# Optimization experiments

Hardware: AMD Instinct MI355X
Metric: run time of the kernel (lower is better)

Reference implementation:

```python
import jax, jax.numpy as jnp
import numpy as np

N_NODES = 50000


def _sage_conv(x, src, dst, Wl, Wr, b):
    # mean aggregation of source-node features onto targets (PyG SAGEConv, aggr='mean')
    msg = x[src]                                              # [E, d]
    agg = jax.ops.segment_sum(msg, dst, num_segments=N_NODES)  # [N, d]
    cnt = jax.ops.segment_sum(jnp.ones((src.shape[0],), x.dtype), dst, num_segments=N_NODES)
    mean = agg / jnp.maximum(cnt, 1.0)[:, None]
    return mean @ Wl + x @ Wr + b


def _layer_norm(x, g, b, eps=1e-5):
    mu = jnp.mean(x, axis=-1, keepdims=True)
    var = jnp.var(x, axis=-1, keepdims=True)
    return (x - mu) * jax.lax.rsqrt(var + eps) * g + b


def setup_inputs() -> dict:
    key = jax.random.key(0)
    ks = jax.random.split(key, 10)
    d_in, d_h, d_out = 128, 128, 2
    scale_h = 1.0 / np.sqrt(d_in)
    x = jax.random.normal(ks[0], (N_NODES, d_in), jnp.float32)
    edge_index = jax.random.randint(ks[1], (2, 800000), 0, N_NODES, dtype=jnp.int64)
    return {
        "x": x,
        "edge_index": edge_index,
        "W1l": jax.random.normal(ks[2], (d_in, d_h), jnp.float32) * scale_h,
        "W1r": jax.random.normal(ks[3], (d_in, d_h), jnp.float32) * scale_h,
        "b1": jnp.zeros((d_h,), jnp.float32),
        "ln1_g": jnp.ones((d_h,), jnp.float32),
        "ln1_b": jnp.zeros((d_h,), jnp.float32),
        "W2l": jax.random.normal(ks[4], (d_h, d_h), jnp.float32) * scale_h,
        "W2r": jax.random.normal(ks[5], (d_h, d_h), jnp.float32) * scale_h,
        "b2": jnp.zeros((d_h,), jnp.float32),
        "ln2_g": jnp.ones((d_h,), jnp.float32),
        "ln2_b": jnp.zeros((d_h,), jnp.float32),
        "W3l": jax.random.normal(ks[6], (d_h, d_out), jnp.float32) * scale_h,
        "W3r": jax.random.normal(ks[7], (d_h, d_out), jnp.float32) * scale_h,
        "b3": jnp.zeros((d_out,), jnp.float32),
    }


def reference(x, edge_index, W1l, W1r, b1, ln1_g, ln1_b, W2l, W2r, b2, ln2_g, ln2_b, W3l, W3r, b3):
    src, dst = edge_index[0], edge_index[1]
    h = _sage_conv(x, src, dst, W1l, W1r, b1)
    h = jax.nn.relu(_layer_norm(h, ln1_g, ln1_b))
    h = _sage_conv(h, src, dst, W2l, W2r, b2)
    h = jax.nn.relu(_layer_norm(h, ln2_g, ln2_b))
    return _sage_conv(h, src, dst, W3l, W3r, b3)
```

## Files before the change

kernel.cpp:

```cpp
#include <hip/hip_runtime.h>

#define N_NODES 50000
#define CAP 64
#define NBK 196
#define BCAP2 4608
#define EPB 4096
#define PB ((int)0xAAAAAAAA)

#define SLS ((size_t)N_NODES * 32)

typedef unsigned int uint;
typedef unsigned short ushort;
typedef __attribute__((ext_vector_type(8))) short bf16x8;
typedef __attribute__((ext_vector_type(4))) float f32x4;

__device__ inline float bf2f(uint u) { u <<= 16; return __builtin_bit_cast(float, u); }
__device__ inline ushort f2bf(float f) {
    uint u = __builtin_bit_cast(uint, f);
    u = (u + 0x7fffu + ((u >> 16) & 1u)) >> 16;
    return (ushort)u;
}


__global__ __launch_bounds__(256) void k_prep(
    const int* __restrict__ src, const int* __restrict__ dst, int E,
    int* __restrict__ bcnt, uint* __restrict__ bstage,
    const float* __restrict__ x, ushort* __restrict__ Xb, int n8,
    const float* __restrict__ W1l, const float* __restrict__ W1r, ushort* __restrict__ Wp1,
    const float* __restrict__ W2l, const float* __restrict__ W2r, ushort* __restrict__ Wp2,
    int bBin, int bC) {
    __shared__ uint recs[EPB];
    __shared__ int hist[NBK], base[NBK], cursor[NBK], gbase[NBK];
    __shared__ int ws[4];
    int b = blockIdx.x, t = threadIdx.x;
    if (b < bBin) {
        int i0 = b * EPB;
        for (int i = t; i < NBK; i += 256) hist[i] = 0;
        __syncthreads();
        uint r[16];
#pragma unroll
        for (int k = 0; k < 16; ++k) {
            int i = i0 + k * 256 + t;
            if (i < E) {
                int s = src[i], d = dst[i];
                r[k] = ((uint)s << 16) | (uint)d;
                atomicAdd(&hist[d >> 8], 1);
            } else r[k] = 0xffffffffu;
        }
        __syncthreads();
        int lane = t & 63, w = t >> 6;
        int v = (t < NBK) ? hist[t] : 0;
        int xsc = v;
#pragma unroll
        for (int o = 1; o < 64; o <<= 1) {
            int y = __shfl_up(xsc, o, 64);
            if (lane >= o) xsc += y;
        }
        if (lane == 63) ws[w] = xsc;
        __syncthreads();
        int add = 0;
        for (int k = 0; k < 4; ++k)
            if (k < w) add += ws[k];
        if (t < NBK) { base[t] = xsc - v + add; cursor[t] = xsc - v + add; }
        __syncthreads();
#pragma unroll
        for (int k = 0; k < 16; ++k) {
            if (r[k] != 0xffffffffu) {
                int bk = (int)((r[k] & 0xffffu) >> 8);
                int pos = atomicAdd(&cursor[bk], 1);
                recs[pos] = r[k];
            }
        }
        __syncthreads();
        for (int i = t; i < NBK; i += 256) {
            int h = hist[i];
            gbase[i] = h ? (atomicAdd(&bcnt[i], h) - PB) : 0;
        }
        __syncthreads();
        int mblk = min(E - i0, EPB);
        for (int i = t; i < mblk; i += 256) {
            uint rr = recs[i];
            int bk = (int)((rr & 0xffffu) >> 8);
            int pos = gbase[bk] + (i - base[bk]);
            if (pos < BCAP2) bstage[(size_t)bk * BCAP2 + pos] = rr;
        }
    } else if (b < bBin + bC) {
        int i = (b - bBin) * 256 + t;
        if (i < n8) {
            int node = i >> 4, f8 = i & 15;
            const float4* xp = (const float4*)(x + (size_t)node * 128 + f8 * 8);
            float4 v0 = xp[0], v1 = xp[1];
            uint4 o;
            o.x = (uint)f2bf(v0.x) | ((uint)f2bf(v0.y) << 16);
            o.y = (uint)f2bf(v0.z) | ((uint)f2bf(v0.w) << 16);
            o.z = (uint)f2bf(v1.x) | ((uint)f2bf(v1.y) << 16);
            o.w = (uint)f2bf(v1.z) | ((uint)f2bf(v1.w) << 16);
            *(uint4*)(Xb + (size_t)(f8 >> 2) * SLS + (size_t)node * 32 + (f8 & 3) * 8) = o;
        }
    } else if (b < bBin + bC + 128) {
        int idx = (b - bBin - bC) * 256 + t;
        int k = idx >> 7, n = idx & 127;
        float v = (k < 128) ? W1l[k * 128 + n] : W1r[(k - 128) * 128 + n];
        Wp1[((k >> 3) << 10) + (n << 3) + (k & 7)] = f2bf(v);
    } else {
        int idx = (b - bBin - bC - 128) * 256 + t;
        int k = idx >> 7, n = idx & 127;
        float v = (k < 128) ? W2l[k * 128 + n] : W2r[(k - 128) * 128 + n];
        Wp2[((k >> 3) << 10) + (n << 3) + (k & 7)] = f2bf(v);
    }
}


__global__ __launch_bounds__(256) void k_csr_build(const int* __restrict__ bcnt,
                                                   const uint* __restrict__ bstage,
                                                   int* __restrict__ cnt,
                                                   ushort* __restrict__ csr, int N) {
    __shared__ int lcnt[256];
    __shared__ ushort lcsr[256 * CAP];
    int b = blockIdx.x, t = threadIdx.x;
    lcnt[t] = 0;
    __syncthreads();
    int m = min(bcnt[b] - PB, BCAP2);
    const uint* st = bstage + (size_t)b * BCAP2;
    for (int i = t; i < m; i += 256) {
        uint rr = st[i];
        int local = rr & 255;
        int slot = atomicAdd(&lcnt[local], 1);
        if (slot < CAP) lcsr[local * CAP + slot] = (ushort)(rr >> 16);
    }
    __syncthreads();
    uint4* d4 = (uint4*)(csr + (size_t)b * 256 * CAP);
    const uint4* s4 = (const uint4*)lcsr;
    for (int i = t; i < 256 * CAP * 2 / 16; i += 256) d4[i] = s4[i];
    int node = b * 256 + t;
    if (node < N) cnt[node] = min(lcnt[t], CAP);
}


__global__ __launch_bounds__(256) void k_agg(const ushort* __restrict__ X,
                                             const int* __restrict__ cnt,
                                             const ushort* __restrict__ csr,
                                             ushort* __restrict__ M, int N) {
    int slice = blockIdx.x & 3;
    int nb = blockIdx.x >> 2;
    int lane = threadIdx.x & 63, wave = threadIdx.x >> 6;
    int es = lane >> 2, fl = lane & 3;
    int node = nb * 64 + wave * 16 + es;
    int end = (node < N) ? cnt[node] : 0;
    int md = end;
    md = max(md, __shfl_xor(md, 4));
    md = max(md, __shfl_xor(md, 8));
    md = max(md, __shfl_xor(md, 16));
    md = max(md, __shfl_xor(md, 32));
    const ushort* rp = csr + (size_t)node * CAP;
    const ushort* Xs = X + (size_t)slice * SLS + fl * 8;
    float a0 = 0.f, a1 = 0.f, a2 = 0.f, a3 = 0.f;
    float a4 = 0.f, a5 = 0.f, a6 = 0.f, a7 = 0.f;
#pragma unroll 4
    for (int e = 0; e < md; ++e) {
        if (e < end) {
            int s = rp[e];
            uint4 v = *(const uint4*)(Xs + (size_t)s * 32);
            a0 += bf2f(v.x); a1 += bf2f(v.x >> 16);
            a2 += bf2f(v.y); a3 += bf2f(v.y >> 16);
            a4 += bf2f(v.z); a5 += bf2f(v.z >> 16);
            a6 += bf2f(v.w); a7 += bf2f(v.w >> 16);
        }
    }
    if (node < N) {
        float inv = 1.0f / (float)max(end, 1);
        uint4 o;
        o.x = (uint)f2bf(a0 * inv) | ((uint)f2bf(a1 * inv) << 16);
        o.y = (uint)f2bf(a2 * inv) | ((uint)f2bf(a3 * inv) << 16);
        o.z = (uint)f2bf(a4 * inv) | ((uint)f2bf(a5 * inv) << 16);
        o.w = (uint)f2bf(a6 * inv) | ((uint)f2bf(a7 * inv) << 16);
        *(uint4*)(M + (size_t)slice * SLS + (size_t)node * 32 + fl * 8) = o;
    }
}


__global__ __launch_bounds__(256, 2) void k_gemm_ln_relu(
    const ushort* __restrict__ Mb, const ushort* __restrict__ Xb,
    const ushort* __restrict__ Wp, const float* __restrict__ bias,
    const float* __restrict__ g, const float* __restrict__ bb,
    ushort* __restrict__ H, int N,
    const float* __restrict__ W3l, const float* __restrict__ W3r,
    const float* __restrict__ b3, float* __restrict__ tb, float* __restrict__ rb) {
    __shared__ ushort sW[256 * 128];
    int tid = threadIdx.x;
    int wave = tid >> 6, lane = tid & 63;
    int l15 = lane & 15, q = lane >> 4;
    int rowBase = blockIdx.x * 64 + wave * 16;
    int arow = rowBase + l15;
    if (arow >= N) arow = N - 1;

    {
        const uint4* wsrc = (const uint4*)Wp;
        uint4* wdst = (uint4*)sW;
#pragma unroll
        for (int i = 0; i < 16; ++i) wdst[i * 256 + tid] = wsrc[i * 256 + tid];
    }

    f32x4 acc[8];
#pragma unroll
    for (int t = 0; t < 8; ++t) acc[t] = (f32x4){0.f, 0.f, 0.f, 0.f};

    const ushort* aM = Mb + (size_t)arow * 32 + q * 8;
    const ushort* aX = Xb + (size_t)arow * 32 + q * 8;
    __syncthreads();
    const ushort* wq = sW + q * 1024 + l15 * 8;

#pragma unroll
    for (int s = 0; s < 8; ++s) {
        bf16x8 a = (s < 4) ? *(const bf16x8*)(aM + (size_t)s * SLS)
                           : *(const bf16x8*)(aX + (size_t)(s - 4) * SLS);
        const ushort* wbase = wq + s * 4096;
#pragma unroll
        for (int t = 0; t < 8; ++t) {
            bf16x8 b = *(const bf16x8*)(wbase + t * 128);
            acc[t] = __builtin_amdgcn_mfma_f32_16x16x32_bf16(a, b, acc[t], 0, 0, 0);
        }
    }

    const bool doProj = (tb != nullptr);
    float gj[8], bbj[8], bj[8];
    float wl0[8], wl1[8], wr0[8], wr1[8];
#pragma unroll
    for (int t = 0; t < 8; ++t) {
        int col = t * 16 + l15;
        gj[t] = g[col]; bbj[t] = bb[col]; bj[t] = bias[col];
    }
    if (doProj) {
#pragma unroll
        for (int t = 0; t < 8; ++t) {
            int col = t * 16 + l15;
            float2 a = *(const float2*)(W3l + col * 2);
            float2 c2 = *(const float2*)(W3r + col * 2);
            wl0[t] = a.x; wl1[t] = a.y; wr0[t] = c2.x; wr1[t] = c2.y;
        }
    }

#pragma unroll
    for (int r = 0; r < 4; ++r) {
        float c[8];
        float s = 0.f, ss = 0.f;
#pragma unroll
        for (int t = 0; t < 8; ++t) {
            c[t] = acc[t][r] + bj[t];
            s += c[t];
            ss += c[t] * c[t];
        }
        s += __shfl_xor(s, 1); ss += __shfl_xor(ss, 1);
        s += __shfl_xor(s, 2); ss += __shfl_xor(ss, 2);
        s += __shfl_xor(s, 4); ss += __shfl_xor(ss, 4);
        s += __shfl_xor(s, 8); ss += __shfl_xor(ss, 8);
        float mu = s * (1.0f / 128.0f);
        float var = ss * (1.0f / 128.0f) - mu * mu;
        float rsig = rsqrtf(var + 1e-5f);
        int node = rowBase + q * 4 + r;
        float y[8];
#pragma unroll
        for (int t = 0; t < 8; ++t) {
            float v = (c[t] - mu) * rsig * gj[t] + bbj[t];
            y[t] = fmaxf(v, 0.f);
        }
        if (!doProj) {
            if (node < N) {
                ushort* hp = H + (size_t)node * 32;
#pragma unroll
                for (int t = 0; t < 8; ++t)
                    hp[(size_t)(t >> 1) * SLS + (t & 1) * 16 + l15] = f2bf(y[t]);
            }
        } else {
            float t0 = 0.f, t1 = 0.f, r0 = 0.f, r1 = 0.f;
#pragma unroll
            for (int t = 0; t < 8; ++t) {
                t0 += y[t] * wl0[t];
                t1 += y[t] * wl1[t];
                r0 += y[t] * wr0[t];
                r1 += y[t] * wr1[t];
            }
#pragma unroll
            for (int o = 1; o < 16; o <<= 1) {
                t0 += __shfl_xor(t0, o);
                t1 += __shfl_xor(t1, o);
                r0 += __shfl_xor(r0, o);
                r1 += __shfl_xor(r1, o);
            }
            if (l15 == 0 && node < N) {
                tb[node * 2 + 0] = t0;
                tb[node * 2 + 1] = t1;
                rb[node * 2 + 0] = r0 + b3[0];
                rb[node * 2 + 1] = r1 + b3[1];
            }
        }
    }
}


__global__ __launch_bounds__(256) void k_final(const float* __restrict__ t, const float* __restrict__ r,
                                               const int* __restrict__ cnt, const ushort* __restrict__ csr,
                                               float* __restrict__ out, int N) {
    int n = blockIdx.x * blockDim.x + threadIdx.x;
    if (n >= N) return;
    int end = cnt[n];
    const ushort* row = csr + (size_t)n * CAP;
    float a0 = 0.f, a1 = 0.f, b0 = 0.f, b1 = 0.f;
    int e = 0;
    for (; e + 3 < end; e += 4) {
        float2 v0 = *(const float2*)(t + row[e] * 2);
        float2 v1 = *(const float2*)(t + row[e + 1] * 2);
        float2 v2 = *(const float2*)(t + row[e + 2] * 2);
        float2 v3 = *(const float2*)(t + row[e + 3] * 2);
        a0 += v0.x + v1.x; a1 += v0.y + v1.y;
        b0 += v2.x + v3.x; b1 += v2.y + v3.y;
    }
    for (; e < end; ++e) {
        float2 v = *(const float2*)(t + row[e] * 2);
        a0 += v.x; a1 += v.y;
    }
    a0 += b0; a1 += b1;
    float inv = 1.0f / (float)max(end, 1);
    out[n * 2 + 0] = a0 * inv + r[n * 2 + 0];
    out[n * 2 + 1] = a1 * inv + r[n * 2 + 1];
}


extern "C" void kernel_launch(void* const* d_in, const int* in_sizes, int n_in,
                              void* d_out, int out_size, void* d_ws, size_t ws_size,
                              hipStream_t stream) {
    const float* x   = (const float*)d_in[0];
    const int* eidx  = (const int*)d_in[1];
    const float* W1l = (const float*)d_in[2];
    const float* W1r = (const float*)d_in[3];
    const float* b1  = (const float*)d_in[4];
    const float* g1  = (const float*)d_in[5];
    const float* bb1 = (const float*)d_in[6];
    const float* W2l = (const float*)d_in[7];
    const float* W2r = (const float*)d_in[8];
    const float* b2  = (const float*)d_in[9];
    const float* g2  = (const float*)d_in[10];
    const float* bb2 = (const float*)d_in[11];
    const float* W3l = (const float*)d_in[12];
    const float* W3r = (const float*)d_in[13];
    const float* b3  = (const float*)d_in[14];
    float* out = (float*)d_out;

    const int N = N_NODES;
    const int E = in_sizes[1] / 2;
    const int* src = eidx;
    const int* dst = eidx + E;

    char* ws = (char*)d_ws;
    size_t off = 0;
    auto alloc = [&](size_t bytes) -> char* {
        char* p = ws + off;
        off += (bytes + 255) & ~(size_t)255;
        return p;
    };
    int* bcnt    = (int*)alloc((size_t)NBK * sizeof(int));
    uint* bstage = (uint*)alloc((size_t)NBK * BCAP2 * sizeof(uint));
    int* cnt     = (int*)alloc((size_t)N * sizeof(int));
    ushort* csr  = (ushort*)alloc((size_t)NBK * 256 * CAP * sizeof(ushort));
    ushort* Xb   = (ushort*)alloc((size_t)N * 128 * sizeof(ushort));
    ushort* Mb   = (ushort*)alloc((size_t)N * 128 * sizeof(ushort));
    ushort* Hb   = (ushort*)alloc((size_t)N * 128 * sizeof(ushort));
    ushort* Wp1  = (ushort*)alloc((size_t)256 * 128 * sizeof(ushort));
    ushort* Wp2  = (ushort*)alloc((size_t)256 * 128 * sizeof(ushort));
    float* tbuf  = (float*)alloc((size_t)N * 2 * sizeof(float));
    float* rbuf  = (float*)alloc((size_t)N * 2 * sizeof(float));

    const int n8 = N * 16;
    const int bBin = (E + EPB - 1) / EPB;
    const int bC = (n8 + 255) / 256;

    k_prep<<<bBin + bC + 256, 256, 0, stream>>>(src, dst, E, bcnt, bstage, x, Xb, n8,
                                                W1l, W1r, Wp1, W2l, W2r, Wp2, bBin, bC);
    k_csr_build<<<NBK, 256, 0, stream>>>(bcnt, bstage, cnt, csr, N);

    const int aggGrid = 4 * ((N + 63) / 64);
    k_agg<<<aggGrid, 256, 0, stream>>>(Xb, cnt, csr, Mb, N);
    k_gemm_ln_relu<<<(N + 63) / 64, 256, 0, stream>>>(Mb, Xb, Wp1, b1, g1, bb1, Hb, N,
                                                      nullptr, nullptr, nullptr, nullptr, nullptr);
    k_agg<<<aggGrid, 256, 0, stream>>>(Hb, cnt, csr, Mb, N);
    k_gemm_ln_relu<<<(N + 63) / 64, 256, 0, stream>>>(Mb, Hb, Wp2, b2, g2, bb2, nullptr, N,
                                                      W3l, W3r, b3, tbuf, rbuf);
    k_final<<<(N + 255) / 256, 256, 0, stream>>>(tbuf, rbuf, cnt, csr, out, N);
}
```

Before: 251.9 us.

## Split each node's neighbor list across four lanes in mean aggregation

```diff
diff --git a/kernel.cpp b/kernel.cpp
--- a/kernel.cpp
+++ b/kernel.cpp
@@ -8,11 +8,13 @@
 #define PB ((int)0xAAAAAAAA)
 
 #define SLS ((size_t)N_NODES * 32)
+#define RS 72
 
 typedef unsigned int uint;
 typedef unsigned short ushort;
 typedef __attribute__((ext_vector_type(8))) short bf16x8;
 typedef __attribute__((ext_vector_type(4))) float f32x4;
+typedef __attribute__((ext_vector_type(4))) uint u32x4;
 
 __device__ inline float bf2f(uint u) { u <<= 16; return __builtin_bit_cast(float, u); }
 __device__ inline ushort f2bf(float f) {
@@ -141,40 +143,68 @@
                                              const int* __restrict__ cnt,
                                              const ushort* __restrict__ csr,
                                              ushort* __restrict__ M, int N) {
+    __shared__ ushort srow[16 * RS];
+    __shared__ int scnt[16];
     int slice = blockIdx.x & 3;
     int nb = blockIdx.x >> 2;
-    int lane = threadIdx.x & 63, wave = threadIdx.x >> 6;
-    int es = lane >> 2, fl = lane & 3;
-    int node = nb * 64 + wave * 16 + es;
-    int end = (node < N) ? cnt[node] : 0;
-    int md = end;
-    md = max(md, __shfl_xor(md, 4));
-    md = max(md, __shfl_xor(md, 8));
-    md = max(md, __shfl_xor(md, 16));
-    md = max(md, __shfl_xor(md, 32));
-    const ushort* rp = csr + (size_t)node * CAP;
+    int node0 = nb * 16;
+    int t = threadIdx.x;
+    if (t < 128) {
+        int ln = t >> 3, c = t & 7;
+        u32x4 v = __builtin_nontemporal_load(
+            (const u32x4*)(csr + (size_t)(node0 + ln) * CAP + c * 8));
+        *(u32x4*)(srow + ln * RS + c * 8) = v;
+        if (c == 0) scnt[ln] = (node0 + ln < N) ? cnt[node0 + ln] : 0;
+    }
+    __syncthreads();
+    int lane = t & 63, wave = t >> 6;
+    int nl = lane >> 4;
+    int es = (lane >> 2) & 3;
+    int fl = lane & 3;
+    int ln = wave * 4 + nl;
+    int node = node0 + ln;
+    int deg = scnt[ln];
+    const ushort* rp = srow + ln * RS;
     const ushort* Xs = X + (size_t)slice * SLS + fl * 8;
     float a0 = 0.f, a1 = 0.f, a2 = 0.f, a3 = 0.f;
     float a4 = 0.f, a5 = 0.f, a6 = 0.f, a7 = 0.f;
-#pragma unroll 4
-    for (int e = 0; e < md; ++e) {
-        if (e < end) {
-            int s = rp[e];
-            uint4 v = *(const uint4*)(Xs + (size_t)s * 32);
-            a0 += bf2f(v.x); a1 += bf2f(v.x >> 16);
-            a2 += bf2f(v.y); a3 += bf2f(v.y >> 16);
-            a4 += bf2f(v.z); a5 += bf2f(v.z >> 16);
-            a6 += bf2f(v.w); a7 += bf2f(v.w >> 16);
-        }
-    }
-    if (node < N) {
-        float inv = 1.0f / (float)max(end, 1);
-        uint4 o;
+    int e = es;
+    for (; e + 4 < deg; e += 8) {
+        int s0 = rp[e], s1 = rp[e + 4];
+        uint4 v0 = *(const uint4*)(Xs + (size_t)s0 * 32);
+        uint4 v1 = *(const uint4*)(Xs + (size_t)s1 * 32);
+        a0 += bf2f(v0.x) + bf2f(v1.x);
+        a1 += bf2f(v0.x >> 16) + bf2f(v1.x >> 16);
+        a2 += bf2f(v0.y) + bf2f(v1.y);
+        a3 += bf2f(v0.y >> 16) + bf2f(v1.y >> 16);
+        a4 += bf2f(v0.z) + bf2f(v1.z);
+        a5 += bf2f(v0.z >> 16) + bf2f(v1.z >> 16);
+        a6 += bf2f(v0.w) + bf2f(v1.w);
+        a7 += bf2f(v0.w >> 16) + bf2f(v1.w >> 16);
+    }
+    if (e < deg) {
+        uint4 v = *(const uint4*)(Xs + (size_t)rp[e] * 32);
+        a0 += bf2f(v.x); a1 += bf2f(v.x >> 16);
+        a2 += bf2f(v.y); a3 += bf2f(v.y >> 16);
+        a4 += bf2f(v.z); a5 += bf2f(v.z >> 16);
+        a6 += bf2f(v.w); a7 += bf2f(v.w >> 16);
+    }
+    a0 += __shfl_xor(a0, 4); a1 += __shfl_xor(a1, 4);
+    a2 += __shfl_xor(a2, 4); a3 += __shfl_xor(a3, 4);
+    a4 += __shfl_xor(a4, 4); a5 += __shfl_xor(a5, 4);
+    a6 += __shfl_xor(a6, 4); a7 += __shfl_xor(a7, 4);
+    a0 += __shfl_xor(a0, 8); a1 += __shfl_xor(a1, 8);
+    a2 += __shfl_xor(a2, 8); a3 += __shfl_xor(a3, 8);
+    a4 += __shfl_xor(a4, 8); a5 += __shfl_xor(a5, 8);
+    a6 += __shfl_xor(a6, 8); a7 += __shfl_xor(a7, 8);
+    if (es == 0 && node < N) {
+        float inv = 1.0f / (float)max(deg, 1);
+        u32x4 o;
         o.x = (uint)f2bf(a0 * inv) | ((uint)f2bf(a1 * inv) << 16);
         o.y = (uint)f2bf(a2 * inv) | ((uint)f2bf(a3 * inv) << 16);
         o.z = (uint)f2bf(a4 * inv) | ((uint)f2bf(a5 * inv) << 16);
         o.w = (uint)f2bf(a6 * inv) | ((uint)f2bf(a7 * inv) << 16);
-        *(uint4*)(M + (size_t)slice * SLS + (size_t)node * 32 + fl * 8) = o;
+        __builtin_nontemporal_store(o, (u32x4*)(M + (size_t)slice * SLS + (size_t)node * 32 + fl * 8));
     }
 }
 
@@ -378,7 +408,7 @@
                                                 W1l, W1r, Wp1, W2l, W2r, Wp2, bBin, bC);
     k_csr_build<<<NBK, 256, 0, stream>>>(bcnt, bstage, cnt, csr, N);
 
-    const int aggGrid = 4 * ((N + 63) / 64);
+    const int aggGrid = 4 * ((N + 15) / 16);
     k_agg<<<aggGrid, 256, 0, stream>>>(Xb, cnt, csr, Mb, N);
     k_gemm_ln_relu<<<(N + 63) / 64, 256, 0, stream>>>(Mb, Xb, Wp1, b1, g1, bb1, Hb, N,
                                                       nullptr, nullptr, nullptr, nullptr, nullptr);
```

Result: faster. 223.0 us (-11.5%).
